# Optimization experiments

Hardware: AMD Instinct MI355X
Metric: run time of the kernel (lower is better)

The kernel has to match this reference:

```python
import jax, jax.numpy as jnp
import numpy as np

NEG_FILL = -999999.0  # sentinel used by the original torch code when masking a channel


def setup_inputs() -> dict:
    key = jax.random.key(0)
    M = jax.random.normal(key, (64, 512, 28, 28), dtype=jnp.float32)
    return {"M": M}


def _dis_loss(M):
    # M: (b, c, h, w). Squared distance from each pixel to the per-map argmax, weighted by M.
    b, c, h, w = M.shape
    Mm = M.reshape(b * c, h, w)
    ind = jnp.argmax(Mm.reshape(b * c, h * w), axis=1)  # flat argmax per map
    indy = ind // w
    indx = ind % w
    y = jnp.arange(h)
    x = jnp.arange(w)
    dy2 = (indy[:, None, None] - y[None, :, None]) ** 2  # (bc, h, 1)
    dx2 = (indx[:, None, None] - x[None, None, :]) ** 2  # (bc, 1, w)
    dist_sq = (dy2 + dx2).astype(M.dtype)  # (bc, h, w)
    return jnp.mean(dist_sq * Mm)


def _div_loss(M):
    # Leave-one-out channel max times each channel, via a single top-2 over channels
    # (equivalent to the O(C^2) clone+max loop in the original).
    b, c, h, w = M.shape
    Mt = jnp.transpose(M, (0, 2, 3, 1))  # (b, h, w, c)
    vals, idxs = jax.lax.top_k(Mt, 2)    # (b, h, w, 2)
    ch = jnp.arange(c)
    # loo[..., c] = max over channels != c
    loo = jnp.where(ch[None, None, None, :] == idxs[..., :1], vals[..., 1:2], vals[..., :1])
    # Original caps the masked channel at -999999; only matters if all other channels < -999999.
    loo = jnp.maximum(loo, NEG_FILL)
    return jnp.mean(loo * Mt)


def reference(M):
    dis_loss = _dis_loss(M)
    div_loss = _div_loss(M)
    return (dis_loss, div_loss)
```

## Files before the change

kernel.cpp:

```cpp
#include <hip/hip_runtime.h>
#include <math.h>

#define BB 64
#define CC 512
#define HWP 784
#define NF4 196
#define NCHUNK 16
#define NPIX4 12544
#define PLANE4 200704
#define DIS_SLOTS 4096
#define DIV_SLOTS 196
#define NEG_FILL -999999.0f
#define NTOT 25690112.0

static __device__ __forceinline__ unsigned sortable(float v) {
  unsigned b = __float_as_uint(v);
  return (b & 0x80000000u) ? ~b : (b | 0x80000000u);
}
static __device__ __forceinline__ void top2(float v, float& v1, float& v2) {
  float lo = fminf(v, v1);
  v1 = fmaxf(v1, v);
  v2 = fmaxf(v2, lo);
}
static __device__ __forceinline__ void mergev(float& v1, float& v2, float b1, float b2) {
  float lo = fminf(v1, b1);
  v1 = fmaxf(v1, b1);
  v2 = fmaxf(lo, fmaxf(v2, b2));
}
static __device__ __forceinline__ void mergev4(float4& v1, float4& v2, float4 b1, float4 b2) {
  mergev(v1.x, v2.x, b1.x, b2.x);
  mergev(v1.y, v2.y, b1.y, b2.y);
  mergev(v1.z, v2.z, b1.z, b2.z);
  mergev(v1.w, v2.w, b1.w, b2.w);
}

__global__ __launch_bounds__(256)
void fused_kernel(const float* __restrict__ M,
    double* __restrict__ slots, float4* __restrict__ wsV1, float4* __restrict__ wsV2,
    float4* __restrict__ wsS, unsigned* __restrict__ counter) {
  const int lane  = threadIdx.x & 63;
  const int w     = threadIdx.x >> 6;
  const int chunk = blockIdx.x;
  const int b     = blockIdx.y;
  if (chunk == 0 && b == 0 && threadIdx.x == 0) *counter = 0u;

  const float* base = M + ((size_t)b * CC + chunk * 32 + w * 8) * HWP;

  float s0[8], sy[8], sx[8], bv[8];
  int bi[8];
  #pragma unroll
  for (int c = 0; c < 8; ++c) { s0[c]=0.f; sy[c]=0.f; sx[c]=0.f; bv[c]=-INFINITY; bi[c]=0; }
  float srr = 0.f;

  __shared__ float4 lm[4][3][NF4];

  auto process = [&](int f) {
    const int y  = f / 7;
    const float fy  = (float)y;
    const float fx0 = (float)((f - y * 7) * 4);
    const float fx1 = fx0 + 1.f, fx2 = fx0 + 2.f, fx3 = fx0 + 3.f;
    const float fyy = fy * fy;
    const float rr0 = fyy + fx0*fx0, rr1 = fyy + fx1*fx1;
    const float rr2 = fyy + fx2*fx2, rr3 = fyy + fx3*fx3;
    const int pxb = f * 4;

    float4 d[8];
    #pragma unroll
    for (int c = 0; c < 8; ++c)
      d[c] = *(const float4*)(base + c * HWP + pxb);

    const float NI = -INFINITY;
    float4 v1 = make_float4(NI, NI, NI, NI);
    float4 v2 = v1;
    float4 S  = make_float4(0.f, 0.f, 0.f, 0.f);

    #pragma unroll
    for (int c = 0; c < 8; ++c) {
      const float a0 = d[c].x, a1 = d[c].y, a2 = d[c].z, a3 = d[c].w;
      const float sum4 = (a0 + a1) + (a2 + a3);
      s0[c] += sum4;
      sy[c] = fmaf(sum4, fy, sy[c]);
      sx[c] = fmaf(a0, fx0, sx[c]); sx[c] = fmaf(a1, fx1, sx[c]);
      sx[c] = fmaf(a2, fx2, sx[c]); sx[c] = fmaf(a3, fx3, sx[c]);
      srr = fmaf(a0, rr0, srr); srr = fmaf(a1, rr1, srr);
      srr = fmaf(a2, rr2, srr); srr = fmaf(a3, rr3, srr);
      if (a0 > bv[c]) { bv[c] = a0; bi[c] = pxb;     }
      if (a1 > bv[c]) { bv[c] = a1; bi[c] = pxb + 1; }
      if (a2 > bv[c]) { bv[c] = a2; bi[c] = pxb + 2; }
      if (a3 > bv[c]) { bv[c] = a3; bi[c] = pxb + 3; }
      top2(a0, v1.x, v2.x); S.x += a0;
      top2(a1, v1.y, v2.y); S.y += a1;
      top2(a2, v1.z, v2.z); S.z += a2;
      top2(a3, v1.w, v2.w); S.w += a3;
    }
    lm[w][0][f] = v1; lm[w][1][f] = v2; lm[w][2][f] = S;
  };

  #pragma unroll
  for (int k = 0; k < 3; ++k) process(lane + 64 * k);
  if (lane < 4) process(192 + lane);

  double dis_acc = (double)srr;
  #pragma unroll
  for (int c = 0; c < 8; ++c) {
    unsigned long long key =
        ((unsigned long long)sortable(bv[c]) << 32) | (unsigned)(~bi[c]);
    #pragma unroll
    for (int off = 1; off < 64; off <<= 1) {
      unsigned long long o = __shfl_xor(key, off);
      key = (key > o) ? key : o;
    }
    const int px = (int)(~((unsigned)key));
    const int iy = px / 28;
    const int ix = px - iy * 28;
    dis_acc += (double)s0[c] * (double)(iy * iy + ix * ix)
             - 2.0 * ((double)sy[c] * (double)iy + (double)sx[c] * (double)ix);
  }
  #pragma unroll
  for (int off = 32; off >= 1; off >>= 1)
    dis_acc += __shfl_down(dis_acc, off);
  if (lane == 0)
    slots[((b * NCHUNK + chunk) << 2) | w] = dis_acc;

  __syncthreads();
  const int t = threadIdx.x;
  if (t < NF4) {
    float4 mv1 = lm[0][0][t], mv2 = lm[0][1][t], mS = lm[0][2][t];
    #pragma unroll
    for (int ww = 1; ww < 4; ++ww) {
      mergev4(mv1, mv2, lm[ww][0][t], lm[ww][1][t]);
      float4 bS = lm[ww][2][t];
      mS.x += bS.x; mS.y += bS.y; mS.z += bS.z; mS.w += bS.w;
    }
    const int idx = chunk * NPIX4 + b * NF4 + t;
    wsV1[idx] = mv1; wsV2[idx] = mv2; wsS[idx] = mS;
  }
}

__global__ __launch_bounds__(256) void div_merge_kernel(const float4* __restrict__ wsV1,
    const float4* __restrict__ wsV2, const float4* __restrict__ wsS,
    double* __restrict__ slots, unsigned* __restrict__ counter,
    float* __restrict__ out) {
  const int t = threadIdx.x, lane = t & 63, w = t >> 6;
  const int g = blockIdx.x * 64 + lane;

  float4 a1[4], a2[4], aS[4];
  #pragma unroll
  for (int c = 0; c < 4; ++c) {
    const int idx = (w * 4 + c) * NPIX4 + g;
    a1[c] = wsV1[idx]; a2[c] = wsV2[idx]; aS[c] = wsS[idx];
  }
  float4 v1 = a1[0], v2 = a2[0], S = aS[0];
  #pragma unroll
  for (int c = 1; c < 4; ++c) {
    mergev4(v1, v2, a1[c], a2[c]);
    S.x += aS[c].x; S.y += aS[c].y; S.z += aS[c].z; S.w += aS[c].w;
  }
  __shared__ float4 sm[4][3][64];
  sm[w][0][lane] = v1; sm[w][1][lane] = v2; sm[w][2][lane] = S;
  __syncthreads();

  if (t < 64) {
    v1 = sm[0][0][t]; v2 = sm[0][1][t]; S = sm[0][2][t];
    #pragma unroll
    for (int ww = 1; ww < 4; ++ww) {
      mergev4(v1, v2, sm[ww][0][t], sm[ww][1][t]);
      float4 bS = sm[ww][2][t];
      S.x += bS.x; S.y += bS.y; S.z += bS.z; S.w += bS.w;
    }
    double contrib =
        (double)fmaxf(v1.x, NEG_FILL) * ((double)S.x - (double)v1.x) + (double)fmaxf(v2.x, NEG_FILL) * (double)v1.x
      + (double)fmaxf(v1.y, NEG_FILL) * ((double)S.y - (double)v1.y) + (double)fmaxf(v2.y, NEG_FILL) * (double)v1.y
      + (double)fmaxf(v1.z, NEG_FILL) * ((double)S.z - (double)v1.z) + (double)fmaxf(v2.z, NEG_FILL) * (double)v1.z
      + (double)fmaxf(v1.w, NEG_FILL) * ((double)S.w - (double)v1.w) + (double)fmaxf(v2.w, NEG_FILL) * (double)v1.w;
    #pragma unroll
    for (int off = 32; off >= 1; off >>= 1)
      contrib += __shfl_down(contrib, off);
    if (t == 0)
      slots[DIS_SLOTS + blockIdx.x] = contrib;
  }

  __shared__ unsigned ticket_s;
  __threadfence();
  __syncthreads();
  if (t == 0) ticket_s = atomicAdd(counter, 1u);
  __syncthreads();
  if (ticket_s == DIV_SLOTS - 1) {
    __threadfence();
    double dis = 0.0;
    #pragma unroll
    for (int i = 0; i < 16; ++i) dis += slots[t + (i << 8)];
    double dv = (t < DIV_SLOTS) ? slots[DIS_SLOTS + t] : 0.0;
    #pragma unroll
    for (int off = 32; off >= 1; off >>= 1) {
      dis += __shfl_down(dis, off);
      dv  += __shfl_down(dv,  off);
    }
    __shared__ double pd[4], pv[4];
    if (lane == 0) { pd[w] = dis; pv[w] = dv; }
    __syncthreads();
    if (t == 0) {
      out[0] = (float)((pd[0] + pd[1] + pd[2] + pd[3]) / NTOT);
      out[1] = (float)((pv[0] + pv[1] + pv[2] + pv[3]) / NTOT);
    }
  }
}

extern "C" void kernel_launch(void* const* d_in, const int* in_sizes, int n_in,
                              void* d_out, int out_size, void* d_ws, size_t ws_size,
                              hipStream_t stream) {
  const float* M = (const float*)d_in[0];
  double*   slots   = (double*)d_ws;
  unsigned* counter = (unsigned*)((char*)d_ws + 40960);
  float4*   planes  = (float4*)((char*)d_ws + 65536);
  float4* wsV1 = planes;
  float4* wsV2 = planes + PLANE4;
  float4* wsS  = planes + 2 * (size_t)PLANE4;
  fused_kernel<<<dim3(NCHUNK, BB), 256, 0, stream>>>(M, slots, wsV1, wsV2, wsS, counter);
  div_merge_kernel<<<DIV_SLOTS, 256, 0, stream>>>(wsV1, wsV2, wsS, slots, counter,
                                                  (float*)d_out);
}
```

Before: 48.42 us.

## Split fused kernel over 8 wavefronts with 4 channels each and staged merges

Doubles the fused kernel's block to 512 threads so each wavefront handles 4 channels instead of 8. The per-pixel top-2 and sum partials are merged through smaller per-iteration shared buffers, with separate thread groups reducing (v1,v2) and S. Tail lanes now run masked fake iterations, and per-wave distance slots double in number. The aim is more memory-level parallelism and fewer registers per thread, at the cost of eight __syncthreads per block and more shared-memory merge passes.

```diff
diff --git a/kernel.cpp b/kernel.cpp
--- a/kernel.cpp
+++ b/kernel.cpp
@@ -8,7 +8,7 @@
 #define NCHUNK 16
 #define NPIX4 12544
 #define PLANE4 200704
-#define DIS_SLOTS 4096
+#define DIS_SLOTS 8192
 #define DIV_SLOTS 196
 #define NEG_FILL -999999.0f
 #define NTOT 25690112.0
@@ -34,28 +34,35 @@
   mergev(v1.w, v2.w, b1.w, b2.w);
 }
 
-__global__ __launch_bounds__(256)
+__global__ __launch_bounds__(512)
 void fused_kernel(const float* __restrict__ M,
     double* __restrict__ slots, float4* __restrict__ wsV1, float4* __restrict__ wsV2,
     float4* __restrict__ wsS, unsigned* __restrict__ counter) {
-  const int lane  = threadIdx.x & 63;
-  const int w     = threadIdx.x >> 6;
+  const int t     = threadIdx.x;
+  const int lane  = t & 63;
+  const int w     = t >> 6;
   const int chunk = blockIdx.x;
   const int b     = blockIdx.y;
-  if (chunk == 0 && b == 0 && threadIdx.x == 0) *counter = 0u;
-
-  const float* base = M + ((size_t)b * CC + chunk * 32 + w * 8) * HWP;
-
-  float s0[8], sy[8], sx[8], bv[8];
-  int bi[8];
-  #pragma unroll
-  for (int c = 0; c < 8; ++c) { s0[c]=0.f; sy[c]=0.f; sx[c]=0.f; bv[c]=-INFINITY; bi[c]=0; }
+  if (chunk == 0 && b == 0 && t == 0) *counter = 0u;
+
+  const float4* base4 =
+      (const float4*)(M + ((size_t)b * CC + chunk * 32 + w * 4) * HWP);
+
+  float s0[4], sy[4], sx[4], bv[4];
+  int bi[4];
+  #pragma unroll
+  for (int c = 0; c < 4; ++c) { s0[c]=0.f; sy[c]=0.f; sx[c]=0.f; bv[c]=-INFINITY; bi[c]=0; }
   float srr = 0.f;
 
-  __shared__ float4 lm[4][3][NF4];
-
-  auto process = [&](int f) {
-    const int y  = f / 7;
+  __shared__ float4 sv1[8][64], sv2[8][64], sS[8][64];
+
+  #pragma unroll
+  for (int k = 0; k < 4; ++k) {
+    const bool tail = (k == 3);
+    const int  f    = tail ? (192 + (lane & 3)) : (lane + 64 * k);
+    const bool fake = tail && (lane >= 4);
+
+    const int y = f / 7;
     const float fy  = (float)y;
     const float fx0 = (float)((f - y * 7) * 4);
     const float fx1 = fx0 + 1.f, fx2 = fx0 + 2.f, fx3 = fx0 + 3.f;
@@ -64,10 +71,9 @@
     const float rr2 = fyy + fx2*fx2, rr3 = fyy + fx3*fx3;
     const int pxb = f * 4;
 
-    float4 d[8];
-    #pragma unroll
-    for (int c = 0; c < 8; ++c)
-      d[c] = *(const float4*)(base + c * HWP + pxb);
+    float4 d[4];
+    #pragma unroll
+    for (int c = 0; c < 4; ++c) d[c] = base4[c * NF4 + f];
 
     const float NI = -INFINITY;
     float4 v1 = make_float4(NI, NI, NI, NI);
@@ -75,8 +81,11 @@
     float4 S  = make_float4(0.f, 0.f, 0.f, 0.f);
 
     #pragma unroll
-    for (int c = 0; c < 8; ++c) {
-      const float a0 = d[c].x, a1 = d[c].y, a2 = d[c].z, a3 = d[c].w;
+    for (int c = 0; c < 4; ++c) {
+      float a0 = d[c].x, a1 = d[c].y, a2 = d[c].z, a3 = d[c].w;
+      if (fake) { a0 = a1 = a2 = a3 = 0.f; }
+      const float q0 = fake ? NI : a0, q1 = fake ? NI : a1;
+      const float q2 = fake ? NI : a2, q3 = fake ? NI : a3;
       const float sum4 = (a0 + a1) + (a2 + a3);
       s0[c] += sum4;
       sy[c] = fmaf(sum4, fy, sy[c]);
@@ -84,25 +93,41 @@
       sx[c] = fmaf(a2, fx2, sx[c]); sx[c] = fmaf(a3, fx3, sx[c]);
       srr = fmaf(a0, rr0, srr); srr = fmaf(a1, rr1, srr);
       srr = fmaf(a2, rr2, srr); srr = fmaf(a3, rr3, srr);
-      if (a0 > bv[c]) { bv[c] = a0; bi[c] = pxb;     }
-      if (a1 > bv[c]) { bv[c] = a1; bi[c] = pxb + 1; }
-      if (a2 > bv[c]) { bv[c] = a2; bi[c] = pxb + 2; }
-      if (a3 > bv[c]) { bv[c] = a3; bi[c] = pxb + 3; }
-      top2(a0, v1.x, v2.x); S.x += a0;
-      top2(a1, v1.y, v2.y); S.y += a1;
-      top2(a2, v1.z, v2.z); S.z += a2;
-      top2(a3, v1.w, v2.w); S.w += a3;
-    }
-    lm[w][0][f] = v1; lm[w][1][f] = v2; lm[w][2][f] = S;
-  };
-
-  #pragma unroll
-  for (int k = 0; k < 3; ++k) process(lane + 64 * k);
-  if (lane < 4) process(192 + lane);
+      if (q0 > bv[c]) { bv[c] = q0; bi[c] = pxb;     }
+      if (q1 > bv[c]) { bv[c] = q1; bi[c] = pxb + 1; }
+      if (q2 > bv[c]) { bv[c] = q2; bi[c] = pxb + 2; }
+      if (q3 > bv[c]) { bv[c] = q3; bi[c] = pxb + 3; }
+      top2(q0, v1.x, v2.x); S.x += a0;
+      top2(q1, v1.y, v2.y); S.y += a1;
+      top2(q2, v1.z, v2.z); S.z += a2;
+      top2(q3, v1.w, v2.w); S.w += a3;
+    }
+    if (!fake) { sv1[w][lane] = v1; sv2[w][lane] = v2; sS[w][lane] = S; }
+    __syncthreads();
+
+    const int glim = tail ? 4 : 64;
+    if (t < glim) {
+      float4 mv1 = sv1[0][t], mv2 = sv2[0][t];
+      #pragma unroll
+      for (int ww = 1; ww < 8; ++ww) mergev4(mv1, mv2, sv1[ww][t], sv2[ww][t]);
+      const int idx = chunk * NPIX4 + b * NF4 + k * 64 + t;
+      wsV1[idx] = mv1; wsV2[idx] = mv2;
+    } else if (t >= 64 && t < 64 + glim) {
+      const int g = t - 64;
+      float4 mS = sS[0][g];
+      #pragma unroll
+      for (int ww = 1; ww < 8; ++ww) {
+        float4 bS = sS[ww][g];
+        mS.x += bS.x; mS.y += bS.y; mS.z += bS.z; mS.w += bS.w;
+      }
+      wsS[chunk * NPIX4 + b * NF4 + k * 64 + g] = mS;
+    }
+    __syncthreads();
+  }
 
   double dis_acc = (double)srr;
   #pragma unroll
-  for (int c = 0; c < 8; ++c) {
+  for (int c = 0; c < 4; ++c) {
     unsigned long long key =
         ((unsigned long long)sortable(bv[c]) << 32) | (unsigned)(~bi[c]);
     #pragma unroll
@@ -120,21 +145,7 @@
   for (int off = 32; off >= 1; off >>= 1)
     dis_acc += __shfl_down(dis_acc, off);
   if (lane == 0)
-    slots[((b * NCHUNK + chunk) << 2) | w] = dis_acc;
-
-  __syncthreads();
-  const int t = threadIdx.x;
-  if (t < NF4) {
-    float4 mv1 = lm[0][0][t], mv2 = lm[0][1][t], mS = lm[0][2][t];
-    #pragma unroll
-    for (int ww = 1; ww < 4; ++ww) {
-      mergev4(mv1, mv2, lm[ww][0][t], lm[ww][1][t]);
-      float4 bS = lm[ww][2][t];
-      mS.x += bS.x; mS.y += bS.y; mS.z += bS.z; mS.w += bS.w;
-    }
-    const int idx = chunk * NPIX4 + b * NF4 + t;
-    wsV1[idx] = mv1; wsV2[idx] = mv2; wsS[idx] = mS;
-  }
+    slots[((b * NCHUNK + chunk) << 3) | w] = dis_acc;
 }
 
 __global__ __launch_bounds__(256) void div_merge_kernel(const float4* __restrict__ wsV1,
@@ -189,7 +200,7 @@
     __threadfence();
     double dis = 0.0;
     #pragma unroll
-    for (int i = 0; i < 16; ++i) dis += slots[t + (i << 8)];
+    for (int i = 0; i < 32; ++i) dis += slots[t + (i << 8)];
     double dv = (t < DIV_SLOTS) ? slots[DIS_SLOTS + t] : 0.0;
     #pragma unroll
     for (int off = 32; off >= 1; off >>= 1) {
@@ -211,12 +222,12 @@
                               hipStream_t stream) {
   const float* M = (const float*)d_in[0];
   double*   slots   = (double*)d_ws;
-  unsigned* counter = (unsigned*)((char*)d_ws + 40960);
-  float4*   planes  = (float4*)((char*)d_ws + 65536);
+  unsigned* counter = (unsigned*)((char*)d_ws + 67584);
+  float4*   planes  = (float4*)((char*)d_ws + 69632);
   float4* wsV1 = planes;
   float4* wsV2 = planes + PLANE4;
   float4* wsS  = planes + 2 * (size_t)PLANE4;
-  fused_kernel<<<dim3(NCHUNK, BB), 256, 0, stream>>>(M, slots, wsV1, wsV2, wsS, counter);
+  fused_kernel<<<dim3(NCHUNK, BB), 512, 0, stream>>>(M, slots, wsV1, wsV2, wsS, counter);
   div_merge_kernel<<<DIV_SLOTS, 256, 0, stream>>>(wsV1, wsV2, wsS, slots, counter,
                                                   (float*)d_out);
 }
```

Result: slower. 58.09 us (+20.0%).
